# Performance work log

Measured on AMD Instinct MI355X. Metric: run time of the kernel, lower is better.

Reference implementation:

```python
import jax, jax.numpy as jnp
import numpy as np

SDF_W = 7000.0
EIK_W = 600.0
ORI_W = 500.0
NEAR_ORI_W = 10.0
GRADN_W = 200.0
K_NEIGHBORS = 2


def _orientation_sign(query, surface, normals, k=K_NEIGHBORS):
    # Original detaches to numpy for a scipy KDTree query -> stop_gradient here.
    q = jax.lax.stop_gradient(query)       # [Q,3]
    s = jax.lax.stop_gradient(surface)     # [S,3]
    n = jax.lax.stop_gradient(normals)     # [S,3]
    # Brute-force squared distances [Q,S] (GEMM-dominated).
    d2 = (jnp.sum(q * q, axis=-1, keepdims=True)
          - 2.0 * (q @ s.T)
          + jnp.sum(s * s, axis=-1)[None, :])
    _, idx = jax.lax.top_k(-d2, k)         # [Q,k] nearest-neighbor indices
    near_pts = s[idx]                      # [Q,k,3]
    near_nrm = n[idx]                      # [Q,k,3]
    vecs = q[:, None, :] - near_pts        # [Q,k,3]
    dots = jnp.sum(vecs * near_nrm, axis=-1)  # [Q,k]
    return jnp.sign(jnp.mean(dots, axis=1))   # [Q]


def setup_inputs() -> dict:
    key = jax.random.key(0)
    ks = jax.random.split(key, 8)
    N = 16384
    return {
        "manifold_pred": jax.random.normal(ks[0], (N, 1), jnp.float32) * 0.1,
        "manifold_grad": jax.random.normal(ks[1], (N, 3), jnp.float32),
        "nonmanifold_pred": jax.random.normal(ks[2], (N, 1), jnp.float32),
        "near_points_pred": jax.random.normal(ks[3], (N, 1), jnp.float32) * 0.1,
        "surface_points": jax.random.normal(ks[4], (N, 3), jnp.float32),
        "surface_normals": jax.random.normal(ks[5], (N, 3), jnp.float32),
        "off_surface_points": jax.random.normal(ks[6], (N, 3), jnp.float32) * 1.5,
        "near_points": jax.random.normal(ks[7], (N, 3), jnp.float32),
    }


def reference(manifold_pred, manifold_grad, nonmanifold_pred, near_points_pred,
              surface_points, surface_normals, off_surface_points, near_points):
    sdf_loss = jnp.mean(manifold_pred ** 2)
    eikonal_loss = jnp.mean((jnp.linalg.norm(manifold_grad, axis=-1) - 1.0) ** 2)

    signs_off = _orientation_sign(off_surface_points, surface_points, surface_normals)
    orientation_loss = jnp.mean(jax.nn.relu(-nonmanifold_pred * signs_off[:, None]))

    signs_near = _orientation_sign(near_points, surface_points, surface_normals)
    near_surface_orientation_loss = jnp.mean(jax.nn.relu(-near_points_pred * signs_near[:, None]))

    gradient_normal_loss = jnp.mean((manifold_grad - surface_normals) ** 2)

    total = (SDF_W * sdf_loss + EIK_W * eikonal_loss + ORI_W * orientation_loss
             + NEAR_ORI_W * near_surface_orientation_loss + GRADN_W * gradient_normal_loss)
    return (total, sdf_loss, eikonal_loss, orientation_loss,
            near_surface_orientation_loss, gradient_normal_loss)
```

## Files before the change

### kernel.cpp

```cpp
#include <hip/hip_runtime.h>
#include <math.h>

#define SDF_W      7000.0f
#define EIK_W      600.0f
#define ORI_W      500.0f
#define NEAR_ORI_W 10.0f
#define GRADN_W    200.0f

#define TILE   2048
#define NWAVE  8
#define CHK    64
#define WS_STRIDE 512
#define WS_REC 4096


__device__ __forceinline__ float neg_half_norm2(float sx, float sy, float sz) {
    return -0.5f * fmaf(sx, sx, fmaf(sy, sy, sz * sz));
}
__device__ __forceinline__ float score(float qx, float qy, float qz,
                                       float sx, float sy, float sz, float nh) {
    return fmaf(qx, sx, fmaf(qy, sy, fmaf(qz, sz, nh)));
}

__global__ __launch_bounds__(512) void nn_scan(
    const float* __restrict__ offq, const float* __restrict__ nearq,
    const float* __restrict__ surf,
    float* __restrict__ ws, int S, int Qoff, int QT)
{
    __shared__ float4 tile[TILE];
    const int t    = threadIdx.x;
    const int lane = t & 63;
    const int wv   = __builtin_amdgcn_readfirstlane(t >> 6);

    const int qgroup = blockIdx.x >> 1;
    const int shalf  = blockIdx.x & 1;

    const int halfLen = (((S + 1) / 2) + (CHK - 1)) & ~(CHK - 1);
    const int sb = shalf ? (halfLen < S ? halfLen : S) : 0;
    const int se = shalf ? S : (halfLen < S ? halfLen : S);

    const int qA = qgroup * 128 + lane;
    const int qB = qA + 64;
    float qAx = 0.f, qAy = 0.f, qAz = 0.f, qBx = 0.f, qBy = 0.f, qBz = 0.f;
    if (qA < QT) {
        const float* p = (qA < Qoff) ? (offq + 3 * qA) : (nearq + 3 * (qA - Qoff));
        qAx = p[0]; qAy = p[1]; qAz = p[2];
    }
    if (qB < QT) {
        const float* p = (qB < Qoff) ? (offq + 3 * qB) : (nearq + 3 * (qB - Qoff));
        qBx = p[0]; qBy = p[1]; qBz = p[2];
    }

    float M1a = -3.0e38f, M2a = -3.0e38f, M1b = -3.0e38f, M2b = -3.0e38f;
    float P1a = M1a, P2a = M2a, P1b = M1b, P2b = M2b;
    int c1a = 0, c2a = 0, c1b = 0, c2b = 0;

    for (int base = sb; base < se; base += TILE) {
        __syncthreads();
        {
            int p0 = base + t * 4;
            if (p0 + 4 <= se) {
                const float4* g4 = (const float4*)(surf + 3 * p0);
                float4 r0 = g4[0], r1 = g4[1], r2 = g4[2];
                tile[t*4+0] = make_float4(r0.x, r0.y, r0.z, neg_half_norm2(r0.x, r0.y, r0.z));
                tile[t*4+1] = make_float4(r0.w, r1.x, r1.y, neg_half_norm2(r0.w, r1.x, r1.y));
                tile[t*4+2] = make_float4(r1.z, r1.w, r2.x, neg_half_norm2(r1.z, r1.w, r2.x));
                tile[t*4+3] = make_float4(r2.y, r2.z, r2.w, neg_half_norm2(r2.y, r2.z, r2.w));
            } else {
                #pragma unroll
                for (int k = 0; k < 4; ++k) {
                    int p = p0 + k;
                    if (p < se) {
                        float sx = surf[3*p], sy = surf[3*p+1], sz = surf[3*p+2];
                        tile[t*4+k] = make_float4(sx, sy, sz, neg_half_norm2(sx, sy, sz));
                    } else {
                        tile[t*4+k] = make_float4(0.f, 0.f, 0.f, -3.0e38f);
                    }
                }
            }
        }
        __syncthreads();
        const int lo = wv * (TILE / NWAVE);
        const float4* tp = tile + lo;
        const int ccbase = (base + lo) >> 6;
        #pragma unroll 1
        for (int c4 = 0; c4 < (TILE / NWAVE) / CHK; ++c4) {
            const float4* cp = tp + c4 * CHK;
            #pragma unroll 8
            for (int o = 0; o < CHK; ++o) {
                float4 s4 = cp[o];
                float ga = score(qAx, qAy, qAz, s4.x, s4.y, s4.z, s4.w);
                float ta = fminf(ga, M1a);
                M2a = fmaxf(M2a, ta);
                M1a = fmaxf(M1a, ga);
                float gb = score(qBx, qBy, qBz, s4.x, s4.y, s4.z, s4.w);
                float tb = fminf(gb, M1b);
                M2b = fmaxf(M2b, tb);
                M1b = fmaxf(M1b, gb);
            }
            int cid = ccbase + c4;
            c1a = (M1a != P1a) ? cid : c1a;  P1a = M1a;
            c2a = (M2a != P2a) ? cid : c2a;  P2a = M2a;
            c1b = (M1b != P1b) ? cid : c1b;  P1b = M1b;
            c2b = (M2b != P2b) ? cid : c2b;  P2b = M2b;
        }
    }

    __syncthreads();
    float4* rec = tile;
    rec[wv * 128 + lane]      = make_float4(M1a, M2a, __int_as_float(c1a), __int_as_float(c2a));
    rec[wv * 128 + 64 + lane] = make_float4(M1b, M2b, __int_as_float(c1b), __int_as_float(c2b));
    __syncthreads();
    if (t < 128) {
        float4 r = rec[t];
        float M1 = r.x, M2 = r.y;
        int c1 = __float_as_int(r.z), c2 = __float_as_int(r.w);
        #pragma unroll
        for (int w = 1; w < NWAVE; ++w) {
            float4 a = rec[w * 128 + t];
            float a1 = a.x, a2 = a.y;
            int ac1 = __float_as_int(a.z), ac2 = __float_as_int(a.w);
            if (a1 > M1)      { M2 = M1; c2 = c1; M1 = a1; c1 = ac1; }
            else if (a1 > M2) { M2 = a1; c2 = ac1; }
            if (a2 > M2)      { M2 = a2; c2 = ac2; }
        }
        int gq = qgroup * 128 + t;
        if (gq < QT) {
            ((float4*)(ws + WS_REC))[gq * 2 + shalf] =
                make_float4(M1, M2, __int_as_float(c1), __int_as_float(c2));
        }
    }
}

__device__ __forceinline__ int find_first(const float* __restrict__ surf, int S,
                                          int c, float qx, float qy, float qz,
                                          float target, int exclude)
{
    int j0 = c * CHK;
    int j1 = j0 + CHK; if (j1 > S) j1 = S;
    if (j1 - j0 == CHK) {
        const float4* g4 = (const float4*)(surf + 3 * j0);
        int found = -1;
        #pragma unroll 1
        for (int b = 0; b < CHK / 16 && found < 0; ++b) {
            float4 raw[12];
            #pragma unroll
            for (int k = 0; k < 12; ++k) raw[k] = g4[b * 12 + k];
            const float* f = (const float*)raw;
            #pragma unroll
            for (int p = 0; p < 16; ++p) {
                float sx = f[3*p], sy = f[3*p+1], sz = f[3*p+2];
                float g = score(qx, qy, qz, sx, sy, sz, neg_half_norm2(sx, sy, sz));
                int j = j0 + b * 16 + p;
                if (found < 0 && g == target && j != exclude) found = j;
            }
        }
        return found;
    }
    for (int j = j0; j < j1; ++j) {
        float sx = surf[3*j], sy = surf[3*j+1], sz = surf[3*j+2];
        float g = score(qx, qy, qz, sx, sy, sz, neg_half_norm2(sx, sy, sz));
        if (g == target && j != exclude) return j;
    }
    return -1;
}

__global__ __launch_bounds__(128) void recover_k(
    const float* __restrict__ offq, const float* __restrict__ nearq,
    const float* __restrict__ surf, const float* __restrict__ norms,
    const float* __restrict__ nmpred, const float* __restrict__ nppred,
    const float* __restrict__ mp, const float* __restrict__ mg,
    const float* __restrict__ sn,
    float* __restrict__ ws, int S, int Qoff, int QT, int N)
{
    const int t = threadIdx.x;
    const int q = blockIdx.x * 128 + t;

    float termOri = 0.f, termNori = 0.f;
    if (q < QT) {
        const float4* recs = (const float4*)(ws + WS_REC);
        float4 r0 = recs[q * 2 + 0], r1 = recs[q * 2 + 1];
        float M1 = r0.x, M2 = r0.y;
        int c1 = __float_as_int(r0.z), c2 = __float_as_int(r0.w);
        {
            float a1 = r1.x, a2 = r1.y;
            int ac1 = __float_as_int(r1.z), ac2 = __float_as_int(r1.w);
            if (a1 > M1)      { M2 = M1; c2 = c1; M1 = a1; c1 = ac1; }
            else if (a1 > M2) { M2 = a1; c2 = ac1; }
            if (a2 > M2)      { M2 = a2; c2 = ac2; }
        }
        bool isNear = (q >= Qoff);
        const float* qp = isNear ? (nearq + 3 * (q - Qoff)) : (offq + 3 * q);
        float qx = qp[0], qy = qp[1], qz = qp[2];

        int I1 = find_first(surf, S, c1, qx, qy, qz, M1, -1);
        if (I1 < 0) I1 = 0;
        int I2 = find_first(surf, S, c2, qx, qy, qz, M2, I1);
        if (I2 < 0) I2 = (I1 == 0 && S > 1) ? 1 : 0;

        float d1 = (qx - surf[3*I1]) * norms[3*I1]
                 + (qy - surf[3*I1+1]) * norms[3*I1+1]
                 + (qz - surf[3*I1+2]) * norms[3*I1+2];
        float d2 = (qx - surf[3*I2]) * norms[3*I2]
                 + (qy - surf[3*I2+1]) * norms[3*I2+1]
                 + (qz - surf[3*I2+2]) * norms[3*I2+2];
        float ms = d1 + d2;
        float sgn = (ms > 0.f) ? 1.f : ((ms < 0.f) ? -1.f : 0.f);
        float pred = isNear ? nppred[q - Qoff] : nmpred[q];
        float term = fmaxf(0.f, -pred * sgn);
        termOri  = isNear ? 0.f : term;
        termNori = isNear ? term : 0.f;
    }

    float sdf = 0.f, eik = 0.f, gn = 0.f;
    for (int i = q; i < N; i += QT) {
        float p = mp[i];
        sdf += p * p;
        float gx = mg[3*i], gy = mg[3*i+1], gz = mg[3*i+2];
        float nrm = sqrtf(fmaf(gx, gx, fmaf(gy, gy, gz * gz)));
        float d = nrm - 1.0f;
        eik += d * d;
        float nx = sn[3*i], ny = sn[3*i+1], nz = sn[3*i+2];
        float dx = gx - nx, dy = gy - ny, dz = gz - nz;
        gn += fmaf(dx, dx, fmaf(dy, dy, dz * dz));
    }

    __shared__ float red[5][128];
    red[0][t] = termOri; red[1][t] = termNori;
    red[2][t] = sdf;     red[3][t] = eik;      red[4][t] = gn;
    __syncthreads();
    for (int off = 64; off > 0; off >>= 1) {
        if (t < off) {
            #pragma unroll
            for (int k = 0; k < 5; ++k) red[k][t] += red[k][t + off];
        }
        __syncthreads();
    }
    if (t == 0) {
        #pragma unroll
        for (int k = 0; k < 5; ++k) ws[k * WS_STRIDE + blockIdx.x] = red[k][0];
    }
}

__global__ __launch_bounds__(256) void final_k(
    const float* __restrict__ ws, float* __restrict__ out,
    int N, int RB, int Qoff, int Qnear)
{
    __shared__ float r[5][256];
    int t = threadIdx.x;
    float s[5] = {0.f, 0.f, 0.f, 0.f, 0.f};
    for (int i = t; i < RB; i += 256) {
        #pragma unroll
        for (int k = 0; k < 5; ++k) s[k] += ws[k * WS_STRIDE + i];
    }
    #pragma unroll
    for (int k = 0; k < 5; ++k) r[k][t] = s[k];
    __syncthreads();
    for (int off = 128; off > 0; off >>= 1) {
        if (t < off) {
            #pragma unroll
            for (int k = 0; k < 5; ++k) r[k][t] += r[k][t + off];
        }
        __syncthreads();
    }
    if (t == 0) {
        float orim  = r[0][0] / (float)Qoff;
        float norim = r[1][0] / (float)Qnear;
        float sdfm  = r[2][0] / (float)N;
        float eikm  = r[3][0] / (float)N;
        float gnm   = r[4][0] / (3.0f * (float)N);
        out[0] = SDF_W * sdfm + EIK_W * eikm + ORI_W * orim
               + NEAR_ORI_W * norim + GRADN_W * gnm;
        out[1] = sdfm;
        out[2] = eikm;
        out[3] = orim;
        out[4] = norim;
        out[5] = gnm;
    }
}

extern "C" void kernel_launch(void* const* d_in, const int* in_sizes, int n_in,
                              void* d_out, int out_size, void* d_ws, size_t ws_size,
                              hipStream_t stream)
{
    const float* mp    = (const float*)d_in[0];
    const float* mg    = (const float*)d_in[1];
    const float* nmp   = (const float*)d_in[2];
    const float* npp   = (const float*)d_in[3];
    const float* sp    = (const float*)d_in[4];
    const float* sn    = (const float*)d_in[5];
    const float* offp  = (const float*)d_in[6];
    const float* nearp = (const float*)d_in[7];
    float* out = (float*)d_out;

    const int N     = in_sizes[0];
    const int S     = in_sizes[4] / 3;
    const int Qoff  = in_sizes[2];
    const int Qnear = in_sizes[3];
    const int QT    = Qoff + Qnear;

    float* ws = (float*)d_ws;

    const int qgroups = (QT + 127) / 128;
    const int RB      = (QT + 127) / 128;

    nn_scan<<<qgroups * 2, 512, 0, stream>>>(offp, nearp, sp, ws, S, Qoff, QT);
    recover_k<<<RB, 128, 0, stream>>>(offp, nearp, sp, sn, nmp, npp,
                                      mp, mg, sn, ws, S, Qoff, QT, N);
    final_k<<<1, 256, 0, stream>>>(ws, out, N, RB, Qoff, Qnear);
}
```

Before: 151.5 us.

## Register-block 8 queries per lane with packed FMA and wave-parallel index recovery

```diff
diff --git a/kernel.cpp b/kernel.cpp
--- a/kernel.cpp
+++ b/kernel.cpp
@@ -7,14 +7,17 @@
 #define NEAR_ORI_W 10.0f
 #define GRADN_W    200.0f
 
-#define TILE   2048
+#define TILE   4096
 #define NWAVE  8
+#define QPL    8
 #define CHK    64
 #define WS_STRIDE 512
 #define WS_REC 4096
 
-
-__device__ __forceinline__ float neg_half_norm2(float sx, float sy, float sz) {
+typedef float v2f __attribute__((ext_vector_type(2)));
+
+
+__device__ __forceinline__ float nh2(float sx, float sy, float sz) {
     return -0.5f * fmaf(sx, sx, fmaf(sy, sy, sz * sz));
 }
 __device__ __forceinline__ float score(float qx, float qy, float qz,
@@ -25,56 +28,72 @@
 __global__ __launch_bounds__(512) void nn_scan(
     const float* __restrict__ offq, const float* __restrict__ nearq,
     const float* __restrict__ surf,
-    float* __restrict__ ws, int S, int Qoff, int QT)
+    float* __restrict__ ws, int S, int Qoff, int QT, int splits, int segLen)
 {
     __shared__ float4 tile[TILE];
     const int t    = threadIdx.x;
     const int lane = t & 63;
     const int wv   = __builtin_amdgcn_readfirstlane(t >> 6);
 
-    const int qgroup = blockIdx.x >> 1;
-    const int shalf  = blockIdx.x & 1;
-
-    const int halfLen = (((S + 1) / 2) + (CHK - 1)) & ~(CHK - 1);
-    const int sb = shalf ? (halfLen < S ? halfLen : S) : 0;
-    const int se = shalf ? S : (halfLen < S ? halfLen : S);
-
-    const int qA = qgroup * 128 + lane;
-    const int qB = qA + 64;
-    float qAx = 0.f, qAy = 0.f, qAz = 0.f, qBx = 0.f, qBy = 0.f, qBz = 0.f;
-    if (qA < QT) {
-        const float* p = (qA < Qoff) ? (offq + 3 * qA) : (nearq + 3 * (qA - Qoff));
-        qAx = p[0]; qAy = p[1]; qAz = p[2];
-    }
-    if (qB < QT) {
-        const float* p = (qB < Qoff) ? (offq + 3 * qB) : (nearq + 3 * (qB - Qoff));
-        qBx = p[0]; qBy = p[1]; qBz = p[2];
-    }
-
-    float M1a = -3.0e38f, M2a = -3.0e38f, M1b = -3.0e38f, M2b = -3.0e38f;
-    float P1a = M1a, P2a = M2a, P1b = M1b, P2b = M2b;
-    int c1a = 0, c2a = 0, c1b = 0, c2b = 0;
+    const int qg = blockIdx.x / splits;
+    const int sp = blockIdx.x % splits;
+    const int sb = sp * segLen;
+    int se = sb + segLen; if (se > S) se = S;
+
+    float qx[QPL], qy[QPL], qz[QPL];
+    #pragma unroll
+    for (int k = 0; k < QPL; ++k) {
+        int q = qg * 512 + k * 64 + lane;
+        float x = 0.f, y = 0.f, z = 0.f;
+        if (q < QT) {
+            const float* p = (q < Qoff) ? (offq + 3 * q) : (nearq + 3 * (q - Qoff));
+            x = p[0]; y = p[1]; z = p[2];
+        }
+        qx[k] = x; qy[k] = y; qz[k] = z;
+    }
+    v2f qx2[QPL/2], qy2[QPL/2], qz2[QPL/2];
+    #pragma unroll
+    for (int p = 0; p < QPL/2; ++p) {
+        qx2[p] = (v2f){qx[2*p], qx[2*p+1]};
+        qy2[p] = (v2f){qy[2*p], qy[2*p+1]};
+        qz2[p] = (v2f){qz[2*p], qz[2*p+1]};
+    }
+
+    float M1[QPL], M2[QPL], P1[QPL], P2[QPL];
+    int   c1[QPL], c2[QPL];
+    const int cinit = (sb < S ? sb : 0) >> 6;
+    #pragma unroll
+    for (int k = 0; k < QPL; ++k) {
+        M1[k] = -3.0e38f; M2[k] = -3.0e38f;
+        P1[k] = -3.0e38f; P2[k] = -3.0e38f;
+        c1[k] = cinit;    c2[k] = cinit;
+    }
 
     for (int base = sb; base < se; base += TILE) {
         __syncthreads();
         {
-            int p0 = base + t * 4;
-            if (p0 + 4 <= se) {
-                const float4* g4 = (const float4*)(surf + 3 * p0);
-                float4 r0 = g4[0], r1 = g4[1], r2 = g4[2];
-                tile[t*4+0] = make_float4(r0.x, r0.y, r0.z, neg_half_norm2(r0.x, r0.y, r0.z));
-                tile[t*4+1] = make_float4(r0.w, r1.x, r1.y, neg_half_norm2(r0.w, r1.x, r1.y));
-                tile[t*4+2] = make_float4(r1.z, r1.w, r2.x, neg_half_norm2(r1.z, r1.w, r2.x));
-                tile[t*4+3] = make_float4(r2.y, r2.z, r2.w, neg_half_norm2(r2.y, r2.z, r2.w));
+            int p0 = base + t * 8;
+            float4* dst = tile + t * 8;
+            if (p0 + 8 <= se) {
+                const float4* g4 = (const float4*)(surf + 3 * (size_t)p0);
+                float4 a = g4[0], b = g4[1], c = g4[2], d = g4[3], e = g4[4], f = g4[5];
+                dst[0] = make_float4(a.x, a.y, a.z, nh2(a.x, a.y, a.z));
+                dst[1] = make_float4(a.w, b.x, b.y, nh2(a.w, b.x, b.y));
+                dst[2] = make_float4(b.z, b.w, c.x, nh2(b.z, b.w, c.x));
+                dst[3] = make_float4(c.y, c.z, c.w, nh2(c.y, c.z, c.w));
+                dst[4] = make_float4(d.x, d.y, d.z, nh2(d.x, d.y, d.z));
+                dst[5] = make_float4(d.w, e.x, e.y, nh2(d.w, e.x, e.y));
+                dst[6] = make_float4(e.z, e.w, f.x, nh2(e.z, e.w, f.x));
+                dst[7] = make_float4(f.y, f.z, f.w, nh2(f.y, f.z, f.w));
             } else {
                 #pragma unroll
-                for (int k = 0; k < 4; ++k) {
+                for (int k = 0; k < 8; ++k) {
                     int p = p0 + k;
                     if (p < se) {
                         float sx = surf[3*p], sy = surf[3*p+1], sz = surf[3*p+2];
-                        tile[t*4+k] = make_float4(sx, sy, sz, neg_half_norm2(sx, sy, sz));
+                        dst[k] = make_float4(sx, sy, sz, nh2(sx, sy, sz));
                     } else {
-                        tile[t*4+k] = make_float4(0.f, 0.f, 0.f, -3.0e38f);
+                        dst[k] = make_float4(0.f, 0.f, 0.f, -3.0e38f);
                     }
                 }
             }
@@ -82,121 +101,116 @@
         __syncthreads();
         const int lo = wv * (TILE / NWAVE);
         const float4* tp = tile + lo;
-        const int ccbase = (base + lo) >> 6;
+        const int cidbase = (base + lo) >> 6;
         #pragma unroll 1
-        for (int c4 = 0; c4 < (TILE / NWAVE) / CHK; ++c4) {
-            const float4* cp = tp + c4 * CHK;
+        for (int c = 0; c < (TILE / NWAVE) / CHK; ++c) {
+            const float4* cp = tp + c * CHK;
             #pragma unroll 8
             for (int o = 0; o < CHK; ++o) {
                 float4 s4 = cp[o];
-                float ga = score(qAx, qAy, qAz, s4.x, s4.y, s4.z, s4.w);
-                float ta = fminf(ga, M1a);
-                M2a = fmaxf(M2a, ta);
-                M1a = fmaxf(M1a, ga);
-                float gb = score(qBx, qBy, qBz, s4.x, s4.y, s4.z, s4.w);
-                float tb = fminf(gb, M1b);
-                M2b = fmaxf(M2b, tb);
-                M1b = fmaxf(M1b, gb);
+                v2f sx = (v2f){s4.x, s4.x};
+                v2f sy = (v2f){s4.y, s4.y};
+                v2f sz = (v2f){s4.z, s4.z};
+                v2f sw = (v2f){s4.w, s4.w};
+                #pragma unroll
+                for (int p = 0; p < QPL/2; ++p) {
+                    v2f g = __builtin_elementwise_fma(qx2[p], sx,
+                            __builtin_elementwise_fma(qy2[p], sy,
+                            __builtin_elementwise_fma(qz2[p], sz, sw)));
+                    float ga = g[0], gb = g[1];
+                    M2[2*p]   = __builtin_amdgcn_fmed3f(ga, M1[2*p], M2[2*p]);
+                    M1[2*p]   = fmaxf(M1[2*p], ga);
+                    M2[2*p+1] = __builtin_amdgcn_fmed3f(gb, M1[2*p+1], M2[2*p+1]);
+                    M1[2*p+1] = fmaxf(M1[2*p+1], gb);
+                }
             }
-            int cid = ccbase + c4;
-            c1a = (M1a != P1a) ? cid : c1a;  P1a = M1a;
-            c2a = (M2a != P2a) ? cid : c2a;  P2a = M2a;
-            c1b = (M1b != P1b) ? cid : c1b;  P1b = M1b;
-            c2b = (M2b != P2b) ? cid : c2b;  P2b = M2b;
+            const int cid = cidbase + c;
+            #pragma unroll
+            for (int k = 0; k < QPL; ++k) {
+                c1[k] = (M1[k] != P1[k]) ? cid : c1[k];  P1[k] = M1[k];
+                c2[k] = (M2[k] != P2[k]) ? cid : c2[k];  P2[k] = M2[k];
+            }
         }
     }
 
     __syncthreads();
     float4* rec = tile;
-    rec[wv * 128 + lane]      = make_float4(M1a, M2a, __int_as_float(c1a), __int_as_float(c2a));
-    rec[wv * 128 + 64 + lane] = make_float4(M1b, M2b, __int_as_float(c1b), __int_as_float(c2b));
+    #pragma unroll
+    for (int k = 0; k < QPL; ++k)
+        rec[wv * 512 + k * 64 + lane] =
+            make_float4(M1[k], M2[k], __int_as_float(c1[k]), __int_as_float(c2[k]));
     __syncthreads();
-    if (t < 128) {
+    {
         float4 r = rec[t];
-        float M1 = r.x, M2 = r.y;
-        int c1 = __float_as_int(r.z), c2 = __float_as_int(r.w);
+        float M1m = r.x, M2m = r.y;
+        int C1 = __float_as_int(r.z), C2 = __float_as_int(r.w);
         #pragma unroll
         for (int w = 1; w < NWAVE; ++w) {
-            float4 a = rec[w * 128 + t];
+            float4 a = rec[w * 512 + t];
             float a1 = a.x, a2 = a.y;
             int ac1 = __float_as_int(a.z), ac2 = __float_as_int(a.w);
-            if (a1 > M1)      { M2 = M1; c2 = c1; M1 = a1; c1 = ac1; }
-            else if (a1 > M2) { M2 = a1; c2 = ac1; }
-            if (a2 > M2)      { M2 = a2; c2 = ac2; }
-        }
-        int gq = qgroup * 128 + t;
+            if (a1 > M1m)      { M2m = M1m; C2 = C1; M1m = a1; C1 = ac1; }
+            else if (a1 > M2m) { M2m = a1; C2 = ac1; }
+            if (a2 > M2m)      { M2m = a2; C2 = ac2; }
+        }
+        int gq = qg * 512 + t;
         if (gq < QT) {
-            ((float4*)(ws + WS_REC))[gq * 2 + shalf] =
-                make_float4(M1, M2, __int_as_float(c1), __int_as_float(c2));
-        }
-    }
-}
-
-__device__ __forceinline__ int find_first(const float* __restrict__ surf, int S,
-                                          int c, float qx, float qy, float qz,
-                                          float target, int exclude)
-{
-    int j0 = c * CHK;
-    int j1 = j0 + CHK; if (j1 > S) j1 = S;
-    if (j1 - j0 == CHK) {
-        const float4* g4 = (const float4*)(surf + 3 * j0);
-        int found = -1;
-        #pragma unroll 1
-        for (int b = 0; b < CHK / 16 && found < 0; ++b) {
-            float4 raw[12];
-            #pragma unroll
-            for (int k = 0; k < 12; ++k) raw[k] = g4[b * 12 + k];
-            const float* f = (const float*)raw;
-            #pragma unroll
-            for (int p = 0; p < 16; ++p) {
-                float sx = f[3*p], sy = f[3*p+1], sz = f[3*p+2];
-                float g = score(qx, qy, qz, sx, sy, sz, neg_half_norm2(sx, sy, sz));
-                int j = j0 + b * 16 + p;
-                if (found < 0 && g == target && j != exclude) found = j;
-            }
-        }
-        return found;
-    }
-    for (int j = j0; j < j1; ++j) {
-        float sx = surf[3*j], sy = surf[3*j+1], sz = surf[3*j+2];
-        float g = score(qx, qy, qz, sx, sy, sz, neg_half_norm2(sx, sy, sz));
-        if (g == target && j != exclude) return j;
-    }
-    return -1;
-}
-
-__global__ __launch_bounds__(128) void recover_k(
+            ((float4*)(ws + WS_REC))[(size_t)gq * splits + sp] =
+                make_float4(M1m, M2m, __int_as_float(C1), __int_as_float(C2));
+        }
+    }
+}
+
+__global__ __launch_bounds__(256) void recover_k(
     const float* __restrict__ offq, const float* __restrict__ nearq,
     const float* __restrict__ surf, const float* __restrict__ norms,
     const float* __restrict__ nmpred, const float* __restrict__ nppred,
     const float* __restrict__ mp, const float* __restrict__ mg,
     const float* __restrict__ sn,
-    float* __restrict__ ws, int S, int Qoff, int QT, int N)
+    float* __restrict__ ws, int S, int Qoff, int QT, int N, int splits)
 {
-    const int t = threadIdx.x;
-    const int q = blockIdx.x * 128 + t;
-
-    float termOri = 0.f, termNori = 0.f;
-    if (q < QT) {
-        const float4* recs = (const float4*)(ws + WS_REC);
-        float4 r0 = recs[q * 2 + 0], r1 = recs[q * 2 + 1];
-        float M1 = r0.x, M2 = r0.y;
-        int c1 = __float_as_int(r0.z), c2 = __float_as_int(r0.w);
-        {
-            float a1 = r1.x, a2 = r1.y;
-            int ac1 = __float_as_int(r1.z), ac2 = __float_as_int(r1.w);
-            if (a1 > M1)      { M2 = M1; c2 = c1; M1 = a1; c1 = ac1; }
-            else if (a1 > M2) { M2 = a1; c2 = ac1; }
-            if (a2 > M2)      { M2 = a2; c2 = ac2; }
-        }
-        bool isNear = (q >= Qoff);
+    const int t    = threadIdx.x;
+    const int lane = t & 63;
+    const int wv   = t >> 6;
+    const int gw   = blockIdx.x * 4 + wv;
+    const int NW   = gridDim.x * 4;
+
+    float ori = 0.f, nori = 0.f;
+    for (int q = gw; q < QT; q += NW) {
+        const float4* recs = ((const float4*)(ws + WS_REC)) + (size_t)q * splits;
+        float4 r = recs[0];
+        float M1 = r.x, M2 = r.y;
+        int C1 = __float_as_int(r.z), C2 = __float_as_int(r.w);
+        for (int i = 1; i < splits; ++i) {
+            float4 a = recs[i];
+            float a1 = a.x, a2 = a.y;
+            int ac1 = __float_as_int(a.z), ac2 = __float_as_int(a.w);
+            if (a1 > M1)      { M2 = M1; C2 = C1; M1 = a1; C1 = ac1; }
+            else if (a1 > M2) { M2 = a1; C2 = ac1; }
+            if (a2 > M2)      { M2 = a2; C2 = ac2; }
+        }
+        const bool isNear = (q >= Qoff);
         const float* qp = isNear ? (nearq + 3 * (q - Qoff)) : (offq + 3 * q);
-        float qx = qp[0], qy = qp[1], qz = qp[2];
-
-        int I1 = find_first(surf, S, c1, qx, qy, qz, M1, -1);
-        if (I1 < 0) I1 = 0;
-        int I2 = find_first(surf, S, c2, qx, qy, qz, M2, I1);
-        if (I2 < 0) I2 = (I1 == 0 && S > 1) ? 1 : 0;
+        const float qx = qp[0], qy = qp[1], qz = qp[2];
+
+        int j1 = C1 * CHK + lane;
+        float g1 = -3.0e38f;
+        if (j1 < S) {
+            float sx = surf[3*j1], sy = surf[3*j1+1], sz = surf[3*j1+2];
+            g1 = score(qx, qy, qz, sx, sy, sz, nh2(sx, sy, sz));
+        }
+        unsigned long long mk1 = __ballot(g1 == M1);
+        int I1 = mk1 ? (C1 * CHK + (int)__builtin_ctzll(mk1)) : 0;
+
+        int j2 = C2 * CHK + lane;
+        float g2 = -3.0e38f;
+        if (j2 < S) {
+            float sx = surf[3*j2], sy = surf[3*j2+1], sz = surf[3*j2+2];
+            g2 = score(qx, qy, qz, sx, sy, sz, nh2(sx, sy, sz));
+        }
+        unsigned long long mk2 = __ballot(g2 == M2 && j2 != I1);
+        int I2 = mk2 ? (C2 * CHK + (int)__builtin_ctzll(mk2))
+                     : ((I1 == 0 && S > 1) ? 1 : 0);
 
         float d1 = (qx - surf[3*I1]) * norms[3*I1]
                  + (qy - surf[3*I1+1]) * norms[3*I1+1]
@@ -204,16 +218,17 @@
         float d2 = (qx - surf[3*I2]) * norms[3*I2]
                  + (qy - surf[3*I2+1]) * norms[3*I2+1]
                  + (qz - surf[3*I2+2]) * norms[3*I2+2];
-        float ms = d1 + d2;
+        float ms  = d1 + d2;
         float sgn = (ms > 0.f) ? 1.f : ((ms < 0.f) ? -1.f : 0.f);
         float pred = isNear ? nppred[q - Qoff] : nmpred[q];
         float term = fmaxf(0.f, -pred * sgn);
-        termOri  = isNear ? 0.f : term;
-        termNori = isNear ? term : 0.f;
+        if (isNear) nori += term; else ori += term;
     }
 
     float sdf = 0.f, eik = 0.f, gn = 0.f;
-    for (int i = q; i < N; i += QT) {
+    const int gid = blockIdx.x * 256 + t;
+    const int GT  = gridDim.x * 256;
+    for (int i = gid; i < N; i += GT) {
         float p = mp[i];
         sdf += p * p;
         float gx = mg[3*i], gy = mg[3*i+1], gz = mg[3*i+2];
@@ -225,11 +240,12 @@
         gn += fmaf(dx, dx, fmaf(dy, dy, dz * dz));
     }
 
-    __shared__ float red[5][128];
-    red[0][t] = termOri; red[1][t] = termNori;
-    red[2][t] = sdf;     red[3][t] = eik;      red[4][t] = gn;
+    __shared__ float red[5][256];
+    red[0][t] = (lane == 0) ? ori  : 0.f;
+    red[1][t] = (lane == 0) ? nori : 0.f;
+    red[2][t] = sdf; red[3][t] = eik; red[4][t] = gn;
     __syncthreads();
-    for (int off = 64; off > 0; off >>= 1) {
+    for (int off = 128; off > 0; off >>= 1) {
         if (t < off) {
             #pragma unroll
             for (int k = 0; k < 5; ++k) red[k][t] += red[k][t + off];
@@ -301,11 +317,15 @@
 
     float* ws = (float*)d_ws;
 
-    const int qgroups = (QT + 127) / 128;
-    const int RB      = (QT + 127) / 128;
-
-    nn_scan<<<qgroups * 2, 512, 0, stream>>>(offp, nearp, sp, ws, S, Qoff, QT);
-    recover_k<<<RB, 128, 0, stream>>>(offp, nearp, sp, sn, nmp, npp,
-                                      mp, mg, sn, ws, S, Qoff, QT, N);
+    const int qgroups = (QT + 511) / 512;
+    size_t need4 = (size_t)WS_REC * 4 + (size_t)QT * 4 * 16 + 1024;
+    const int splits = (ws_size >= need4) ? 4 : 2;
+    const int segLen = ((S + splits - 1) / splits + CHK - 1) / CHK * CHK;
+
+    const int RB = 256;
+    nn_scan<<<qgroups * splits, 512, 0, stream>>>(offp, nearp, sp, ws,
+                                                  S, Qoff, QT, splits, segLen);
+    recover_k<<<RB, 256, 0, stream>>>(offp, nearp, sp, sn, nmp, npp,
+                                      mp, mg, sn, ws, S, Qoff, QT, N, splits);
     final_k<<<1, 256, 0, stream>>>(ws, out, N, RB, Qoff, Qnear);
 }
```

New measurement: 197.0 us. 30.0% more time.
